# Kernel optimization log

Hardware: AMD Instinct MI355X
Metric: run time of the kernel (lower is better)

The kernel has to match this reference:

```python
import jax, jax.numpy as jnp
import numpy as np

HEAD = 16
HEAD_DIM = 64


def setup_inputs() -> dict:
    key = jax.random.key(0)
    ks = jax.random.split(key, 6)
    B, S, D = 8, 1024, 1024
    s = 1.0 / np.sqrt(D)
    return {
        "queries": jax.random.normal(ks[0], (B, S, D), jnp.float32),
        "keys": jax.random.normal(ks[1], (B, S, D), jnp.float32),
        "values": jax.random.normal(ks[2], (B, S, D), jnp.float32),
        "Wq": jax.random.normal(ks[3], (D, HEAD * HEAD_DIM), jnp.float32) * s,
        "Wk": jax.random.normal(ks[4], (D, HEAD * HEAD_DIM), jnp.float32) * s,
        "Wv": jax.random.normal(ks[5], (D, HEAD * HEAD_DIM), jnp.float32) * s,
    }


def reference(queries, keys, values, Wq, Wk, Wv):
    B, Sq, _ = queries.shape
    Sk = keys.shape[1]
    # Linear projections: [B, S, H*D]
    q = jnp.einsum("bsd,df->bsf", queries, Wq).reshape(B, Sq, HEAD, HEAD_DIM)
    k = jnp.einsum("bsd,df->bsf", keys, Wk).reshape(B, Sk, HEAD, HEAD_DIM)
    v = jnp.einsum("bsd,df->bsf", values, Wv).reshape(B, Sk, HEAD, HEAD_DIM)
    # Scaled dot-product attention per head (scale uses head_dim, as in source
    scores = jnp.einsum("bqhd,bkhd->bhqk", q, k) / np.sqrt(HEAD_DIM).astype(np.float32)
    attn = jax.nn.softmax(scores, axis=-1)
    out = jnp.einsum("bhqk,bkhd->bqhd", attn, v)  # [B, Sq, H, D]
    # concat heads back on feature axis: [B, Sq, H*D]
    return out.reshape(B, Sq, HEAD * HEAD_DIM)
```

## Files before the change

### kernel.cpp

```cpp
#include <hip/hip_runtime.h>
#include <hip/hip_bf16.h>


typedef __bf16 bf16;
typedef unsigned int uint;
typedef float f32x4 __attribute__((ext_vector_type(4)));
typedef float f32x16 __attribute__((ext_vector_type(16)));
typedef bf16 bf16x8 __attribute__((ext_vector_type(8)));

#define QK_SCALE 0.18033688011112042f

static __device__ __forceinline__ f32x4 mfma16(bf16x8 a, bf16x8 b, f32x4 c) {
    return __builtin_amdgcn_mfma_f32_16x16x32_bf16(a, b, c, 0, 0, 0);
}
static __device__ __forceinline__ f32x16 mfma32(bf16x8 a, bf16x8 b, f32x16 c) {
    return __builtin_amdgcn_mfma_f32_32x32x16_bf16(a, b, c, 0, 0, 0);
}

__global__ __launch_bounds__(256)
void wconv_kernel(const float* __restrict__ Wq, const float* __restrict__ Wk,
                  const float* __restrict__ Wv, bf16* __restrict__ Tq,
                  bf16* __restrict__ Tk, bf16* __restrict__ Tv) {
    const int z = blockIdx.z;
    const float* W = z == 0 ? Wq : (z == 1 ? Wk : Wv);
    bf16* Wt = z == 0 ? Tq : (z == 1 ? Tk : Tv);
    const float sc = z == 0 ? QK_SCALE : 1.0f;
    __shared__ bf16 t[32][33];
    const int tx = threadIdx.x, ty = threadIdx.y;
    const int n0 = blockIdx.x * 32, k0 = blockIdx.y * 32;
#pragma unroll
    for (int i = 0; i < 4; ++i)
        t[ty + i * 8][tx] = (bf16)(W[(size_t)(k0 + ty + i * 8) * 1024 + n0 + tx] * sc);
    __syncthreads();
#pragma unroll
    for (int i = 0; i < 4; ++i)
        Wt[(size_t)(n0 + ty + i * 8) * 1024 + k0 + tx] = t[tx][ty + i * 8];
}

template <int MODE>
__global__ __launch_bounds__(256)
void gemm_proj(const float* __restrict__ X, const bf16* __restrict__ Wt,
               bf16* __restrict__ out) {
    __shared__ bf16 Asub[2][128][40];
    __shared__ bf16 Bsub[2][128][40];
    const int tid = threadIdx.x;
    const int lane = tid & 63;
    const int w = tid >> 6;
    const int m0 = blockIdx.x * 128;
    const int n0 = blockIdx.y * 128;
    const int wm = (w >> 1) * 64;
    const int wn = (w & 1) * 64;
    const int lrow = lane & 15;
    const int lk8 = (lane >> 4) * 8;
    const int lr4 = (lane >> 4) * 4;

    f32x4 acc[4][4];
#pragma unroll
    for (int i = 0; i < 4; ++i)
#pragma unroll
        for (int j = 0; j < 4; ++j)
            acc[i][j] = f32x4{0.f, 0.f, 0.f, 0.f};

    const int srow = tid >> 1;
    const int skh = (tid & 1) * 16;
    const float* xg = X + (size_t)(m0 + srow) * 1024 + skh;
    const bf16* bg = Wt + (size_t)(n0 + srow) * 1024 + skh;

    {
        const float4 f0 = *(const float4*)(xg + 0);
        const float4 f1 = *(const float4*)(xg + 4);
        const float4 f2 = *(const float4*)(xg + 8);
        const float4 f3 = *(const float4*)(xg + 12);
        const bf16x8 b0 = *(const bf16x8*)(bg + 0);
        const bf16x8 b1 = *(const bf16x8*)(bg + 8);
        bf16x8 a0, a1;
        a0[0] = (bf16)f0.x; a0[1] = (bf16)f0.y; a0[2] = (bf16)f0.z; a0[3] = (bf16)f0.w;
        a0[4] = (bf16)f1.x; a0[5] = (bf16)f1.y; a0[6] = (bf16)f1.z; a0[7] = (bf16)f1.w;
        a1[0] = (bf16)f2.x; a1[1] = (bf16)f2.y; a1[2] = (bf16)f2.z; a1[3] = (bf16)f2.w;
        a1[4] = (bf16)f3.x; a1[5] = (bf16)f3.y; a1[6] = (bf16)f3.z; a1[7] = (bf16)f3.w;
        *(bf16x8*)&Asub[0][srow][skh + 0] = a0;
        *(bf16x8*)&Asub[0][srow][skh + 8] = a1;
        *(bf16x8*)&Bsub[0][srow][skh + 0] = b0;
        *(bf16x8*)&Bsub[0][srow][skh + 8] = b1;
    }
    __syncthreads();

    int cur = 0;
    for (int kt = 0; kt < 32; ++kt) {
        float4 f0, f1, f2, f3;
        bf16x8 b0, b1;
        if (kt < 31) {
            const int k0 = (kt + 1) * 32;
            f0 = *(const float4*)(xg + k0 + 0);
            f1 = *(const float4*)(xg + k0 + 4);
            f2 = *(const float4*)(xg + k0 + 8);
            f3 = *(const float4*)(xg + k0 + 12);
            b0 = *(const bf16x8*)(bg + k0 + 0);
            b1 = *(const bf16x8*)(bg + k0 + 8);
        }
        bf16x8 af[4], bfv[4];
#pragma unroll
        for (int i = 0; i < 4; ++i)
            af[i] = *(const bf16x8*)&Asub[cur][wm + i * 16 + lrow][lk8];
#pragma unroll
        for (int j = 0; j < 4; ++j)
            bfv[j] = *(const bf16x8*)&Bsub[cur][wn + j * 16 + lrow][lk8];
#pragma unroll
        for (int i = 0; i < 4; ++i)
#pragma unroll
            for (int j = 0; j < 4; ++j)
                acc[i][j] = mfma16(af[i], bfv[j], acc[i][j]);
        if (kt < 31) {
            bf16x8 a0, a1;
            a0[0] = (bf16)f0.x; a0[1] = (bf16)f0.y; a0[2] = (bf16)f0.z; a0[3] = (bf16)f0.w;
            a0[4] = (bf16)f1.x; a0[5] = (bf16)f1.y; a0[6] = (bf16)f1.z; a0[7] = (bf16)f1.w;
            a1[0] = (bf16)f2.x; a1[1] = (bf16)f2.y; a1[2] = (bf16)f2.z; a1[3] = (bf16)f2.w;
            a1[4] = (bf16)f3.x; a1[5] = (bf16)f3.y; a1[6] = (bf16)f3.z; a1[7] = (bf16)f3.w;
            *(bf16x8*)&Asub[cur ^ 1][srow][skh + 0] = a0;
            *(bf16x8*)&Asub[cur ^ 1][srow][skh + 8] = a1;
            *(bf16x8*)&Bsub[cur ^ 1][srow][skh + 0] = b0;
            *(bf16x8*)&Bsub[cur ^ 1][srow][skh + 8] = b1;
        }
        __syncthreads();
        cur ^= 1;
    }

#pragma unroll
    for (int j = 0; j < 4; ++j) {
        const int n = n0 + wn + j * 16 + lrow;
        const int h = n >> 6, dh = n & 63;
#pragma unroll
        for (int i = 0; i < 4; ++i) {
#pragma unroll
            for (int r = 0; r < 4; ++r) {
                const int m = m0 + wm + i * 16 + lr4 + r;
                const int b = m >> 10, s = m & 1023;
                const bf16 val = (bf16)acc[i][j][r];
                if (MODE == 0)
                    out[((size_t)((b * 16 + h) * 1024 + s)) * 64 + dh] = val;
                else
                    out[((size_t)((b * 16 + h) * 64 + dh)) * 1024 + s] = val;
            }
        }
    }
}

__global__ __launch_bounds__(256)
void attn_kernel(const bf16* __restrict__ Q, const bf16* __restrict__ K,
                 const bf16* __restrict__ Vt, float* __restrict__ out) {
    __shared__ bf16 Ksub[2][64][72];
    __shared__ bf16 Vsub[2][64][72];
    __shared__ float Lsub[4][32];

    const int tid = threadIdx.x, lane = tid & 63, w = tid >> 6;
    const int l31 = lane & 31;
    const int hi = lane >> 5;
    const int lin = blockIdx.x;
    const int xcd = lin & 7;
    const int slot = lin >> 3;
    const int bh = (slot >> 3) * 8 + xcd;
    const int qt = slot & 7;
    const int q0 = qt * 128;
    const size_t base = (size_t)bh << 16;

    bf16x8 qf[4];
    {
        const bf16* qg = Q + base + (size_t)(q0 + w * 32 + l31) * 64 + hi * 8;
#pragma unroll
        for (int ds = 0; ds < 4; ++ds) qf[ds] = *(const bf16x8*)(qg + ds * 16);
    }

    f32x16 acc_o[2];
#pragma unroll
    for (int nf = 0; nf < 2; ++nf)
#pragma unroll
        for (int r = 0; r < 16; ++r) acc_o[nf][r] = 0.f;
    float l_part = 0.f;

    const bf16* kg = K + base + (size_t)(tid >> 2) * 64 + (tid & 3) * 16;
    const bf16* vg = Vt + base + (size_t)(tid >> 2) * 1024 + (tid & 3) * 16;

    {
        const bf16x8 kv0 = *(const bf16x8*)(kg + 0);
        const bf16x8 kv1 = *(const bf16x8*)(kg + 8);
        const bf16x8 vv0 = *(const bf16x8*)(vg + 0);
        const bf16x8 vv1 = *(const bf16x8*)(vg + 8);
        bf16* kd = &Ksub[0][tid >> 2][(tid & 3) * 16];
        bf16* vd = &Vsub[0][tid >> 2][(tid & 3) * 16];
        *(bf16x8*)(kd + 0) = kv0; *(bf16x8*)(kd + 8) = kv1;
        *(bf16x8*)(vd + 0) = vv0; *(bf16x8*)(vd + 8) = vv1;
    }
    __syncthreads();

    int cur = 0;
    for (int t = 0; t < 16; ++t) {
        bf16x8 kv0, kv1, vv0, vv1;
        if (t < 15) {
            const int sn = (t + 1) * 64;
            kv0 = *(const bf16x8*)(kg + sn * 64 + 0);
            kv1 = *(const bf16x8*)(kg + sn * 64 + 8);
            vv0 = *(const bf16x8*)(vg + sn + 0);
            vv1 = *(const bf16x8*)(vg + sn + 8);
        }

        f32x16 sa0, sa1;
#pragma unroll
        for (int r = 0; r < 16; ++r) { sa0[r] = 0.f; sa1[r] = 0.f; }
        __builtin_amdgcn_s_setprio(1);
#pragma unroll
        for (int ds = 0; ds < 4; ++ds) {
            const bf16x8 k0 = *(const bf16x8*)&Ksub[cur][l31][ds * 16 + hi * 8];
            const bf16x8 k1 = *(const bf16x8*)&Ksub[cur][32 + l31][ds * 16 + hi * 8];
            sa0 = mfma32(k0, qf[ds], sa0);
            sa1 = mfma32(k1, qf[ds], sa1);
        }
        __builtin_amdgcn_s_setprio(0);

        float p0[16], p1[16];
#pragma unroll
        for (int r = 0; r < 16; ++r) {
            p0[r] = __builtin_amdgcn_exp2f(sa0[r]);
            p1[r] = __builtin_amdgcn_exp2f(sa1[r]);
            l_part += p0[r] + p1[r];
        }

        uint c0[8], c1[8];
#pragma unroll
        for (int bb = 0; bb < 8; ++bb) {
            union { bf16 h[2]; uint u; } u0, u1;
            u0.h[0] = (bf16)p0[2 * bb]; u0.h[1] = (bf16)p0[2 * bb + 1];
            u1.h[0] = (bf16)p1[2 * bb]; u1.h[1] = (bf16)p1[2 * bb + 1];
            c0[bb] = u0.u; c1[bb] = u1.u;
        }
        constexpr int SA[4] = {0, 1, 4, 5}, SB[4] = {2, 3, 6, 7};
        uint x0[4], x1[4];
#pragma unroll
        for (int j = 0; j < 4; ++j) {
            x0[j] = __shfl_xor(hi ? c0[SA[j]] : c0[SB[j]], 32);
            x1[j] = __shfl_xor(hi ? c1[SA[j]] : c1[SB[j]], 32);
        }
        bf16x8 pf00, pf01, pf10, pf11;
#pragma unroll
        for (int ks2 = 0; ks2 < 2; ++ks2) {
            union { uint u[4]; bf16x8 v; } a0, a1;
#pragma unroll
            for (int e = 0; e < 4; ++e) {
                const int xo = (e & 1) + 2 * ks2;
                const int co = (e & 1) + 4 * ks2;
                if (e < 2) {
                    a0.u[e] = hi ? x0[xo] : c0[co];
                    a1.u[e] = hi ? x1[xo] : c1[co];
                } else {
                    a0.u[e] = hi ? c0[co + 2] : x0[xo];
                    a1.u[e] = hi ? c1[co + 2] : x1[xo];
                }
            }
            if (ks2 == 0) { pf00 = a0.v; pf10 = a1.v; }
            else          { pf01 = a0.v; pf11 = a1.v; }
        }

        __builtin_amdgcn_s_setprio(1);
#pragma unroll
        for (int ks = 0; ks < 4; ++ks) {
            const bf16x8 pa = (ks == 0) ? pf00 : (ks == 1) ? pf01
                            : (ks == 2) ? pf10 : pf11;
#pragma unroll
            for (int nf = 0; nf < 2; ++nf) {
                const bf16x8 vf =
                    *(const bf16x8*)&Vsub[cur][nf * 32 + l31][ks * 16 + hi * 8];
                acc_o[nf] = mfma32(pa, vf, acc_o[nf]);
            }
        }
        __builtin_amdgcn_s_setprio(0);

        if (t < 15) {
            bf16* kd = &Ksub[cur ^ 1][tid >> 2][(tid & 3) * 16];
            bf16* vd = &Vsub[cur ^ 1][tid >> 2][(tid & 3) * 16];
            *(bf16x8*)(kd + 0) = kv0; *(bf16x8*)(kd + 8) = kv1;
            *(bf16x8*)(vd + 0) = vv0; *(bf16x8*)(vd + 8) = vv1;
        }
        __syncthreads();
        cur ^= 1;
    }

    const float l_tot = l_part + __shfl_xor(l_part, 32);
    if (lane < 32) Lsub[w][l31] = l_tot;
    const int b = bh >> 4, hh = bh & 15;
#pragma unroll
    for (int r = 0; r < 16; ++r) {
        const int q = (r & 3) + 8 * (r >> 2) + 4 * hi;
        const float inv = 1.0f / Lsub[w][q];
        const size_t row = (size_t)(b * 1024 + q0 + w * 32 + q) * 1024 + hh * 64;
#pragma unroll
        for (int nf = 0; nf < 2; ++nf)
            out[row + nf * 32 + l31] = acc_o[nf][r] * inv;
    }
}

extern "C" void kernel_launch(void* const* d_in, const int* in_sizes, int n_in,
                              void* d_out, int out_size, void* d_ws, size_t ws_size,
                              hipStream_t stream) {
    (void)in_sizes; (void)n_in; (void)out_size; (void)ws_size;
    const float* queries = (const float*)d_in[0];
    const float* keys    = (const float*)d_in[1];
    const float* values  = (const float*)d_in[2];
    const float* Wq      = (const float*)d_in[3];
    const float* Wk      = (const float*)d_in[4];
    const float* Wv      = (const float*)d_in[5];
    float* out = (float*)d_out;

    bf16* q_ws  = (bf16*)d_ws;
    bf16* k_ws  = q_ws + (size_t)8 * 1024 * 1024;
    bf16* vt_ws = k_ws + (size_t)8 * 1024 * 1024;
    bf16* wt_q  = vt_ws + (size_t)8 * 1024 * 1024;
    bf16* wt_k  = wt_q + (size_t)1024 * 1024;
    bf16* wt_v  = wt_k + (size_t)1024 * 1024;

    wconv_kernel<<<dim3(32, 32, 3), dim3(32, 8), 0, stream>>>(
        Wq, Wk, Wv, wt_q, wt_k, wt_v);

    gemm_proj<0><<<dim3(64, 8), 256, 0, stream>>>(queries, wt_q, q_ws);
    gemm_proj<0><<<dim3(64, 8), 256, 0, stream>>>(keys,    wt_k, k_ws);
    gemm_proj<1><<<dim3(64, 8), 256, 0, stream>>>(values,  wt_v, vt_ws);

    attn_kernel<<<dim3(1024), 256, 0, stream>>>(q_ws, k_ws, vt_ws, out);
}
```

Before: 183.1 us.

## Load K/V fragments directly from global memory instead of staging in LDS

Drops the double-buffered shared-memory K and V tiles and the per-iteration barrier in the attention kernel. Each wave now reads its MFMA operand fragments straight from global memory, relying on L1/L2 to serve the reuse across the four waves. The row-sum accumulator is also split into four partial sums to shorten the dependency chain. The risk is that each wave repeats the global/cache traffic and that there is no explicit prefetch, so load latency may be exposed.

```diff
diff --git a/kernel.cpp b/kernel.cpp
--- a/kernel.cpp
+++ b/kernel.cpp
@@ -148,8 +148,6 @@
 __global__ __launch_bounds__(256)
 void attn_kernel(const bf16* __restrict__ Q, const bf16* __restrict__ K,
                  const bf16* __restrict__ Vt, float* __restrict__ out) {
-    __shared__ bf16 Ksub[2][64][72];
-    __shared__ bf16 Vsub[2][64][72];
     __shared__ float Lsub[4][32];
 
     const int tid = threadIdx.x, lane = tid & 63, w = tid >> 6;
@@ -175,33 +173,15 @@
     for (int nf = 0; nf < 2; ++nf)
 #pragma unroll
         for (int r = 0; r < 16; ++r) acc_o[nf][r] = 0.f;
-    float l_part = 0.f;
-
-    const bf16* kg = K + base + (size_t)(tid >> 2) * 64 + (tid & 3) * 16;
-    const bf16* vg = Vt + base + (size_t)(tid >> 2) * 1024 + (tid & 3) * 16;
-
-    {
-        const bf16x8 kv0 = *(const bf16x8*)(kg + 0);
-        const bf16x8 kv1 = *(const bf16x8*)(kg + 8);
-        const bf16x8 vv0 = *(const bf16x8*)(vg + 0);
-        const bf16x8 vv1 = *(const bf16x8*)(vg + 8);
-        bf16* kd = &Ksub[0][tid >> 2][(tid & 3) * 16];
-        bf16* vd = &Vsub[0][tid >> 2][(tid & 3) * 16];
-        *(bf16x8*)(kd + 0) = kv0; *(bf16x8*)(kd + 8) = kv1;
-        *(bf16x8*)(vd + 0) = vv0; *(bf16x8*)(vd + 8) = vv1;
-    }
-    __syncthreads();
-
-    int cur = 0;
+    float l_acc[4] = {0.f, 0.f, 0.f, 0.f};
+
+    const bf16* kp0 = K + base + (size_t)l31 * 64 + hi * 8;
+    const bf16* kp1 = kp0 + 32 * 64;
+    const bf16* vp0 = Vt + base + (size_t)l31 * 1024 + hi * 8;
+    const bf16* vp1 = vp0 + 32 * 1024;
+
     for (int t = 0; t < 16; ++t) {
-        bf16x8 kv0, kv1, vv0, vv1;
-        if (t < 15) {
-            const int sn = (t + 1) * 64;
-            kv0 = *(const bf16x8*)(kg + sn * 64 + 0);
-            kv1 = *(const bf16x8*)(kg + sn * 64 + 8);
-            vv0 = *(const bf16x8*)(vg + sn + 0);
-            vv1 = *(const bf16x8*)(vg + sn + 8);
-        }
+        const int s0 = t * 64;
 
         f32x16 sa0, sa1;
 #pragma unroll
@@ -209,8 +189,8 @@
         __builtin_amdgcn_s_setprio(1);
 #pragma unroll
         for (int ds = 0; ds < 4; ++ds) {
-            const bf16x8 k0 = *(const bf16x8*)&Ksub[cur][l31][ds * 16 + hi * 8];
-            const bf16x8 k1 = *(const bf16x8*)&Ksub[cur][32 + l31][ds * 16 + hi * 8];
+            const bf16x8 k0 = *(const bf16x8*)(kp0 + (size_t)s0 * 64 + ds * 16);
+            const bf16x8 k1 = *(const bf16x8*)(kp1 + (size_t)s0 * 64 + ds * 16);
             sa0 = mfma32(k0, qf[ds], sa0);
             sa1 = mfma32(k1, qf[ds], sa1);
         }
@@ -221,7 +201,7 @@
         for (int r = 0; r < 16; ++r) {
             p0[r] = __builtin_amdgcn_exp2f(sa0[r]);
             p1[r] = __builtin_amdgcn_exp2f(sa1[r]);
-            l_part += p0[r] + p1[r];
+            l_acc[r & 3] += p0[r] + p1[r];
         }
 
         uint c0[8], c1[8];
@@ -264,25 +244,15 @@
         for (int ks = 0; ks < 4; ++ks) {
             const bf16x8 pa = (ks == 0) ? pf00 : (ks == 1) ? pf01
                             : (ks == 2) ? pf10 : pf11;
-#pragma unroll
-            for (int nf = 0; nf < 2; ++nf) {
-                const bf16x8 vf =
-                    *(const bf16x8*)&Vsub[cur][nf * 32 + l31][ks * 16 + hi * 8];
-                acc_o[nf] = mfma32(pa, vf, acc_o[nf]);
-            }
+            const bf16x8 vf0 = *(const bf16x8*)(vp0 + s0 + ks * 16);
+            const bf16x8 vf1 = *(const bf16x8*)(vp1 + s0 + ks * 16);
+            acc_o[0] = mfma32(pa, vf0, acc_o[0]);
+            acc_o[1] = mfma32(pa, vf1, acc_o[1]);
         }
         __builtin_amdgcn_s_setprio(0);
-
-        if (t < 15) {
-            bf16* kd = &Ksub[cur ^ 1][tid >> 2][(tid & 3) * 16];
-            bf16* vd = &Vsub[cur ^ 1][tid >> 2][(tid & 3) * 16];
-            *(bf16x8*)(kd + 0) = kv0; *(bf16x8*)(kd + 8) = kv1;
-            *(bf16x8*)(vd + 0) = vv0; *(bf16x8*)(vd + 8) = vv1;
-        }
-        __syncthreads();
-        cur ^= 1;
-    }
-
+    }
+
+    float l_part = (l_acc[0] + l_acc[1]) + (l_acc[2] + l_acc[3]);
     const float l_tot = l_part + __shfl_xor(l_part, 32);
     if (lane < 32) Lsub[w][l31] = l_tot;
     const int b = bh >> 4, hh = bh & 15;
```

Measured after the change: 287.2 us. 1.57x slower.
